# Kernel tuning notes

Hardware: AMD Instinct MI355X
Metric: run time of the kernel (lower is better)

## Reference

```python
import jax, jax.numpy as jnp
import numpy as np

N_ENTITIES = 100000
N_EDGES = 1250000
N_RELATIONS = 32
D = 64


def setup_inputs() -> dict:
    key = jax.random.key(0)
    k1, k2, k3, k4 = jax.random.split(key, 4)
    entity_emb = jax.random.normal(k1, (N_ENTITIES, D), dtype=jnp.float32)
    edge_index = jax.random.randint(k2, (2, N_EDGES), 0, N_ENTITIES, dtype=jnp.int64)
    edge_type = jax.random.randint(k3, (N_EDGES,), 0, N_RELATIONS, dtype=jnp.int64)
    weight = jax.random.normal(k4, (N_RELATIONS, D), dtype=jnp.float32)
    return {"entity_emb": entity_emb, "edge_index": edge_index,
            "edge_type": edge_type, "weight": weight}


def reference(entity_emb, edge_index, edge_type, weight):
    n_entities = entity_emb.shape[0]
    head, tail = edge_index[0], edge_index[1]
    # gather tail entity embeddings and relation embeddings, elementwise multiply
    neigh_relation_emb = entity_emb[tail] * weight[edge_type]  # [E, D]
    # scatter_mean by head index
    sums = jax.ops.segment_sum(neigh_relation_emb, head, num_segments=n_entities)
    counts = jax.ops.segment_sum(jnp.ones((head.shape[0],), dtype=entity_emb.dtype),
                                 head, num_segments=n_entities)
    entity_agg = sums / jnp.maximum(counts, 1.0)[:, None]  # empty segments -> 0
    return entity_agg
```

## Files before the change

kernel.cpp:

```cpp
#include <hip/hip_runtime.h>

#define D 64
#define BIN_SHIFT 7
#define BIN_SIZE 128
#define MAX_BINS 1024
#define BINCAP 2560
#define K1_THREADS 512
#define K1_EPT 8
#define K1_EPB (K1_THREADS * K1_EPT)
#define K2_THREADS 512
#define NREL 32


__global__ void __launch_bounds__(K1_THREADS)
bin_sort_kernel(const int* __restrict__ head,
                const int* __restrict__ tail,
                const int* __restrict__ etype,
                int* __restrict__ binCount,
                unsigned* __restrict__ recs,
                int nbins, int n_edges) {
    __shared__ int hist[MAX_BINS];
    __shared__ int pos[MAX_BINS];
    int tid = threadIdx.x;
    for (int b = tid; b < nbins; b += K1_THREADS) hist[b] = 0;
    __syncthreads();

    long blockBase = (long)blockIdx.x * K1_EPB;
    int hv[K1_EPT];
#pragma unroll
    for (int k = 0; k < K1_EPT; k++) {
        long e = blockBase + (long)k * K1_THREADS + tid;
        hv[k] = (e < n_edges) ? head[e] : -1;
        if (hv[k] >= 0) atomicAdd(&hist[hv[k] >> BIN_SHIFT], 1);
    }
    __syncthreads();

    for (int b = tid; b < nbins; b += K1_THREADS) {
        int c = hist[b];
        pos[b] = (c > 0) ? atomicAdd(&binCount[b], c) : 0;
    }
    __syncthreads();

#pragma unroll
    for (int k = 0; k < K1_EPT; k++) {
        int h = hv[k];
        if (h >= 0) {
            long e = blockBase + (long)k * K1_THREADS + tid;
            int b = h >> BIN_SHIFT;
            int r = atomicAdd(&pos[b], 1);
            if (r < BINCAP)
                recs[(long)b * BINCAP + r] =
                    (unsigned)tail[e] | ((unsigned)etype[e] << 17)
                  | ((unsigned)(h & (BIN_SIZE - 1)) << 22);
        }
    }
}

__global__ void __launch_bounds__(K2_THREADS)
aggregate_bin_kernel(const float* __restrict__ emb,
                     const float* __restrict__ weight,
                     const unsigned* __restrict__ recs,
                     const int* __restrict__ binCount,
                     float* __restrict__ out, int n_ent) {
    __shared__ unsigned raw[BINCAP];
    __shared__ unsigned sorted[BINCAP + 16];
    __shared__ float wlds[NREL * D];
    __shared__ int hist[BIN_SIZE];
    __shared__ int off[BIN_SIZE];
    __shared__ int cur[BIN_SIZE];

    int tid = threadIdx.x;
    int b = blockIdx.x;
    int n = min(binCount[b], BINCAP);

    for (int i = tid; i < BINCAP + 16; i += K2_THREADS) sorted[i] = 0u;
    for (int i = tid; i < NREL * D; i += K2_THREADS) wlds[i] = weight[i];
    if (tid < BIN_SIZE) hist[tid] = 0;
    __syncthreads();

    const unsigned* gr = recs + (long)b * BINCAP;
    for (int i = tid; i < n; i += K2_THREADS) {
        unsigned q = gr[i];
        raw[i] = q;
        atomicAdd(&hist[(q >> 22) & 127], 1);
    }
    __syncthreads();

    int v = 0;
    if (tid < BIN_SIZE) { v = hist[tid]; off[tid] = v; }
    __syncthreads();
    for (int s = 1; s < BIN_SIZE; s <<= 1) {
        int x = 0;
        if (tid < BIN_SIZE && tid >= s) x = off[tid - s];
        __syncthreads();
        if (tid < BIN_SIZE) off[tid] += x;
        __syncthreads();
    }
    if (tid < BIN_SIZE) { off[tid] -= v; cur[tid] = off[tid]; }
    __syncthreads();

    for (int i = tid; i < n; i += K2_THREADS) {
        unsigned q = raw[i];
        int p = atomicAdd(&cur[(q >> 22) & 127], 1);
        sorted[p] = q;
    }
    __syncthreads();

    int lane = tid & 63;
    int wave = tid >> 6;
    int g = lane >> 4;
    int c = lane & 15;
    int hbase = b << BIN_SHIFT;

    for (int hl = wave; hl < BIN_SIZE; hl += 8) {
        if (hbase + hl >= n_ent) break;
        int o = off[hl];
        int deg = hist[hl];
        float4 acc = make_float4(0.f, 0.f, 0.f, 0.f);
        for (int i = 0; i < deg; i += 16) {
            int e0 = i + g, e1 = i + 4 + g, e2 = i + 8 + g, e3 = i + 12 + g;
            unsigned q0 = sorted[o + e0];
            unsigned q1 = sorted[o + e1];
            unsigned q2 = sorted[o + e2];
            unsigned q3 = sorted[o + e3];
            float4 v0 = *(const float4*)&emb[(long)(q0 & 0x1FFFF) * D + c * 4];
            float4 v1 = *(const float4*)&emb[(long)(q1 & 0x1FFFF) * D + c * 4];
            float4 v2 = *(const float4*)&emb[(long)(q2 & 0x1FFFF) * D + c * 4];
            float4 v3 = *(const float4*)&emb[(long)(q3 & 0x1FFFF) * D + c * 4];
            float4 w0 = *(const float4*)&wlds[(((q0 >> 17) & 31) << 6) + c * 4];
            float4 w1 = *(const float4*)&wlds[(((q1 >> 17) & 31) << 6) + c * 4];
            float4 w2 = *(const float4*)&wlds[(((q2 >> 17) & 31) << 6) + c * 4];
            float4 w3 = *(const float4*)&wlds[(((q3 >> 17) & 31) << 6) + c * 4];
            float m0 = (e0 < deg) ? 1.f : 0.f;
            float m1 = (e1 < deg) ? 1.f : 0.f;
            float m2 = (e2 < deg) ? 1.f : 0.f;
            float m3 = (e3 < deg) ? 1.f : 0.f;
            acc.x += m0 * v0.x * w0.x; acc.y += m0 * v0.y * w0.y;
            acc.z += m0 * v0.z * w0.z; acc.w += m0 * v0.w * w0.w;
            acc.x += m1 * v1.x * w1.x; acc.y += m1 * v1.y * w1.y;
            acc.z += m1 * v1.z * w1.z; acc.w += m1 * v1.w * w1.w;
            acc.x += m2 * v2.x * w2.x; acc.y += m2 * v2.y * w2.y;
            acc.z += m2 * v2.z * w2.z; acc.w += m2 * v2.w * w2.w;
            acc.x += m3 * v3.x * w3.x; acc.y += m3 * v3.y * w3.y;
            acc.z += m3 * v3.z * w3.z; acc.w += m3 * v3.w * w3.w;
        }
        acc.x += __shfl_xor(acc.x, 16); acc.y += __shfl_xor(acc.y, 16);
        acc.z += __shfl_xor(acc.z, 16); acc.w += __shfl_xor(acc.w, 16);
        acc.x += __shfl_xor(acc.x, 32); acc.y += __shfl_xor(acc.y, 32);
        acc.z += __shfl_xor(acc.z, 32); acc.w += __shfl_xor(acc.w, 32);
        if (g == 0) {
            float inv = 1.f / fmaxf((float)deg, 1.f);
            *(float4*)&out[(long)(hbase + hl) * D + c * 4] =
                make_float4(acc.x * inv, acc.y * inv, acc.z * inv, acc.w * inv);
        }
    }
}

__global__ void fb_scatter(const float* __restrict__ emb, const int* __restrict__ head,
                           const int* __restrict__ tail, const int* __restrict__ etype,
                           const float* __restrict__ weight, float* __restrict__ out,
                           float* __restrict__ cnt, int n_edges) {
    int gtid = blockIdx.x * blockDim.x + threadIdx.x;
    int e = gtid >> 6, lane = threadIdx.x & 63;
    if (e >= n_edges) return;
    int h = head[e], t = tail[e], r = etype[e];
    atomicAdd(&out[(long)h * D + lane], emb[(long)t * D + lane] * weight[r * D + lane]);
    if (lane == 0) atomicAdd(&cnt[h], 1.0f);
}
__global__ void fb_divide(float* __restrict__ out, const float* __restrict__ cnt, int n) {
    int i = blockIdx.x * blockDim.x + threadIdx.x;
    if (i < n) out[i] = out[i] / fmaxf(cnt[i >> 6], 1.0f);
}


extern "C" void kernel_launch(void* const* d_in, const int* in_sizes, int n_in,
                              void* d_out, int out_size, void* d_ws, size_t ws_size,
                              hipStream_t stream) {
    const float* emb    = (const float*)d_in[0];
    const int*   eidx   = (const int*)  d_in[1];
    const int*   etype  = (const int*)  d_in[2];
    const float* weight = (const float*)d_in[3];
    float* out = (float*)d_out;

    int n_edges = in_sizes[2];
    int n_ent   = out_size / D;
    const int* head = eidx;
    const int* tail = eidx + n_edges;

    int nbins = (n_ent + BIN_SIZE - 1) >> BIN_SHIFT;
    size_t need = sizeof(int) * ((size_t)nbins * (BINCAP + 1));
    long mean_load = (n_ent > 0) ? ((long)n_edges * BIN_SIZE / n_ent) : 0;
    bool ok = (n_ent <= 131072) && (nbins <= MAX_BINS) && (ws_size >= need) &&
              (mean_load + 700 <= BINCAP);

    if (ok) {
        int* binCount  = (int*)d_ws;
        unsigned* recs = (unsigned*)(binCount + nbins);

        hipMemsetAsync(binCount, 0, (size_t)nbins * sizeof(int), stream);

        int nblocks = (n_edges + K1_EPB - 1) / K1_EPB;
        bin_sort_kernel<<<nblocks, K1_THREADS, 0, stream>>>(
            head, tail, etype, binCount, recs, nbins, n_edges);

        aggregate_bin_kernel<<<nbins, K2_THREADS, 0, stream>>>(
            emb, weight, recs, binCount, out, n_ent);
    } else {
        float* cnt = (float*)d_ws;
        hipMemsetAsync(out, 0, (size_t)out_size * sizeof(float), stream);
        hipMemsetAsync(cnt, 0, (size_t)n_ent * sizeof(float), stream);
        long tt = (long)n_edges * 64;
        fb_scatter<<<(int)((tt + 255) / 256), 256, 0, stream>>>(
            emb, head, tail, etype, weight, out, cnt, n_edges);
        fb_divide<<<(out_size + 255) / 256, 256, 0, stream>>>(out, cnt, out_size);
    }
}
```

Measured before the change: 158.4 us.

## Stage bin records in LDS for coalesced writes and split aggregation into half-bins

The binning kernel now sorts each block's records by bin in shared memory. It then writes them to global memory contiguously, using a binary search over bin bases, instead of as scattered per-edge stores. The aggregation kernel launches two 256-thread blocks per bin, each handling 64 heads, which doubles the block count for better occupancy. Each wave now processes two heads at once to expose more independent gathers. In exchange, each half-block rescans the whole bin's records, there is an extra LDS prefix scan, and a second capacity limit (HCAP) can push more inputs onto the fallback path.

```diff
diff --git a/kernel.cpp b/kernel.cpp
--- a/kernel.cpp
+++ b/kernel.cpp
@@ -5,10 +5,11 @@
 #define BIN_SIZE 128
 #define MAX_BINS 1024
 #define BINCAP 2560
+#define HCAP 1536
 #define K1_THREADS 512
 #define K1_EPT 8
 #define K1_EPB (K1_THREADS * K1_EPT)
-#define K2_THREADS 512
+#define K2_THREADS 256
 #define NREL 32
 
 
@@ -19,139 +20,211 @@
                 int* __restrict__ binCount,
                 unsigned* __restrict__ recs,
                 int nbins, int n_edges) {
+    __shared__ unsigned srec[K1_EPB];
     __shared__ int hist[MAX_BINS];
-    __shared__ int pos[MAX_BINS];
+    __shared__ int base[MAX_BINS + 1];
+    __shared__ int cur[MAX_BINS];
+    __shared__ int gpos[MAX_BINS];
+    __shared__ int tmp[K1_THREADS];
+
     int tid = threadIdx.x;
-    for (int b = tid; b < nbins; b += K1_THREADS) hist[b] = 0;
+    for (int b = tid; b < MAX_BINS; b += K1_THREADS) hist[b] = 0;
     __syncthreads();
 
     long blockBase = (long)blockIdx.x * K1_EPB;
-    int hv[K1_EPT];
+    int nvalid = (int)(((long)n_edges - blockBase < (long)K1_EPB)
+                       ? ((long)n_edges - blockBase) : (long)K1_EPB);
+
+    unsigned rv[K1_EPT]; int bv[K1_EPT];
 #pragma unroll
     for (int k = 0; k < K1_EPT; k++) {
         long e = blockBase + (long)k * K1_THREADS + tid;
-        hv[k] = (e < n_edges) ? head[e] : -1;
-        if (hv[k] >= 0) atomicAdd(&hist[hv[k] >> BIN_SHIFT], 1);
-    }
+        if (e < n_edges) {
+            int h = head[e];
+            bv[k] = h >> BIN_SHIFT;
+            rv[k] = (unsigned)tail[e] | ((unsigned)etype[e] << 17)
+                  | ((unsigned)(h & (BIN_SIZE - 1)) << 22);
+            atomicAdd(&hist[bv[k]], 1);
+        } else bv[k] = -1;
+    }
+    __syncthreads();
+
+    int s0 = hist[2 * tid], s1 = hist[2 * tid + 1];
+    tmp[tid] = s0 + s1;
+    __syncthreads();
+    for (int s = 1; s < K1_THREADS; s <<= 1) {
+        int x = (tid >= s) ? tmp[tid - s] : 0;
+        __syncthreads();
+        tmp[tid] += x;
+        __syncthreads();
+    }
+    int pairExcl = tmp[tid] - (s0 + s1);
+    base[2 * tid] = pairExcl;      cur[2 * tid] = pairExcl;
+    base[2 * tid + 1] = pairExcl + s0; cur[2 * tid + 1] = pairExcl + s0;
+    if (tid == K1_THREADS - 1) base[MAX_BINS] = tmp[tid];
     __syncthreads();
 
     for (int b = tid; b < nbins; b += K1_THREADS) {
         int c = hist[b];
-        pos[b] = (c > 0) ? atomicAdd(&binCount[b], c) : 0;
+        gpos[b] = (c > 0) ? atomicAdd(&binCount[b], c) : 0;
     }
     __syncthreads();
 
 #pragma unroll
     for (int k = 0; k < K1_EPT; k++) {
-        int h = hv[k];
-        if (h >= 0) {
-            long e = blockBase + (long)k * K1_THREADS + tid;
-            int b = h >> BIN_SHIFT;
-            int r = atomicAdd(&pos[b], 1);
-            if (r < BINCAP)
-                recs[(long)b * BINCAP + r] =
-                    (unsigned)tail[e] | ((unsigned)etype[e] << 17)
-                  | ((unsigned)(h & (BIN_SIZE - 1)) << 22);
-        }
+        if (bv[k] >= 0) {
+            int p = atomicAdd(&cur[bv[k]], 1);
+            srec[p] = rv[k];
+        }
+    }
+    __syncthreads();
+
+    for (int i = tid; i < nvalid; i += K1_THREADS) {
+        int lo = 0, hi = nbins - 1;
+        while (lo < hi) {
+            int mid = (lo + hi + 1) >> 1;
+            if (base[mid] <= i) lo = mid; else hi = mid - 1;
+        }
+        int b = lo;
+        int off = gpos[b] + (i - base[b]);
+        if (off < BINCAP)
+            recs[(long)b * BINCAP + off] = srec[i];
     }
 }
 
 __global__ void __launch_bounds__(K2_THREADS)
-aggregate_bin_kernel(const float* __restrict__ emb,
-                     const float* __restrict__ weight,
-                     const unsigned* __restrict__ recs,
-                     const int* __restrict__ binCount,
-                     float* __restrict__ out, int n_ent) {
-    __shared__ unsigned raw[BINCAP];
-    __shared__ unsigned sorted[BINCAP + 16];
+aggregate_half_kernel(const float* __restrict__ emb,
+                      const float* __restrict__ weight,
+                      const unsigned* __restrict__ recs,
+                      const int* __restrict__ binCount,
+                      float* __restrict__ out, int n_ent) {
+    __shared__ unsigned raw[HCAP];
+    __shared__ unsigned sorted[HCAP + 16];
     __shared__ float wlds[NREL * D];
-    __shared__ int hist[BIN_SIZE];
-    __shared__ int off[BIN_SIZE];
-    __shared__ int cur[BIN_SIZE];
+    __shared__ int hist[64], off[64], cur[64];
+    __shared__ int nh;
 
     int tid = threadIdx.x;
-    int b = blockIdx.x;
+    int b = blockIdx.x >> 1;
+    int half = blockIdx.x & 1;
     int n = min(binCount[b], BINCAP);
 
-    for (int i = tid; i < BINCAP + 16; i += K2_THREADS) sorted[i] = 0u;
+    for (int i = tid; i < HCAP + 16; i += K2_THREADS) sorted[i] = 0u;
     for (int i = tid; i < NREL * D; i += K2_THREADS) wlds[i] = weight[i];
-    if (tid < BIN_SIZE) hist[tid] = 0;
+    if (tid < 64) hist[tid] = 0;
+    if (tid == 0) nh = 0;
     __syncthreads();
 
     const unsigned* gr = recs + (long)b * BINCAP;
     for (int i = tid; i < n; i += K2_THREADS) {
         unsigned q = gr[i];
-        raw[i] = q;
-        atomicAdd(&hist[(q >> 22) & 127], 1);
-    }
-    __syncthreads();
+        int hl = (q >> 22) & 127;
+        if ((hl >> 6) == half) {
+            int p = atomicAdd(&nh, 1);
+            if (p < HCAP) { raw[p] = q; atomicAdd(&hist[hl & 63], 1); }
+        }
+    }
+    __syncthreads();
+    int m = min(nh, HCAP);
 
     int v = 0;
-    if (tid < BIN_SIZE) { v = hist[tid]; off[tid] = v; }
-    __syncthreads();
-    for (int s = 1; s < BIN_SIZE; s <<= 1) {
+    if (tid < 64) { v = hist[tid]; off[tid] = v; }
+    __syncthreads();
+    for (int s = 1; s < 64; s <<= 1) {
         int x = 0;
-        if (tid < BIN_SIZE && tid >= s) x = off[tid - s];
-        __syncthreads();
-        if (tid < BIN_SIZE) off[tid] += x;
-        __syncthreads();
-    }
-    if (tid < BIN_SIZE) { off[tid] -= v; cur[tid] = off[tid]; }
-    __syncthreads();
-
-    for (int i = tid; i < n; i += K2_THREADS) {
+        if (tid < 64 && tid >= s) x = off[tid - s];
+        __syncthreads();
+        if (tid < 64) off[tid] += x;
+        __syncthreads();
+    }
+    if (tid < 64) { off[tid] -= v; cur[tid] = off[tid]; }
+    __syncthreads();
+
+    for (int i = tid; i < m; i += K2_THREADS) {
         unsigned q = raw[i];
-        int p = atomicAdd(&cur[(q >> 22) & 127], 1);
+        int p = atomicAdd(&cur[(q >> 22) & 63], 1);
         sorted[p] = q;
     }
     __syncthreads();
 
-    int lane = tid & 63;
-    int wave = tid >> 6;
-    int g = lane >> 4;
-    int c = lane & 15;
-    int hbase = b << BIN_SHIFT;
-
-    for (int hl = wave; hl < BIN_SIZE; hl += 8) {
-        if (hbase + hl >= n_ent) break;
-        int o = off[hl];
-        int deg = hist[hl];
-        float4 acc = make_float4(0.f, 0.f, 0.f, 0.f);
-        for (int i = 0; i < deg; i += 16) {
+    int lane = tid & 63, wave = tid >> 6;
+    int g = lane >> 4, c = lane & 15;
+    int hbase = (b << BIN_SHIFT) + (half << 6);
+    int cap = m + 15;
+
+    for (int j = 0; j < 16; j += 2) {
+        int hA = wave * 16 + j, hB = hA + 1;
+        int oA = off[hA], dA = hist[hA];
+        int oB = off[hB], dB = hist[hB];
+        float4 aA = make_float4(0.f,0.f,0.f,0.f);
+        float4 aB = make_float4(0.f,0.f,0.f,0.f);
+        int dmax = max(dA, dB);
+        for (int i = 0; i < dmax; i += 16) {
             int e0 = i + g, e1 = i + 4 + g, e2 = i + 8 + g, e3 = i + 12 + g;
-            unsigned q0 = sorted[o + e0];
-            unsigned q1 = sorted[o + e1];
-            unsigned q2 = sorted[o + e2];
-            unsigned q3 = sorted[o + e3];
-            float4 v0 = *(const float4*)&emb[(long)(q0 & 0x1FFFF) * D + c * 4];
-            float4 v1 = *(const float4*)&emb[(long)(q1 & 0x1FFFF) * D + c * 4];
-            float4 v2 = *(const float4*)&emb[(long)(q2 & 0x1FFFF) * D + c * 4];
-            float4 v3 = *(const float4*)&emb[(long)(q3 & 0x1FFFF) * D + c * 4];
-            float4 w0 = *(const float4*)&wlds[(((q0 >> 17) & 31) << 6) + c * 4];
-            float4 w1 = *(const float4*)&wlds[(((q1 >> 17) & 31) << 6) + c * 4];
-            float4 w2 = *(const float4*)&wlds[(((q2 >> 17) & 31) << 6) + c * 4];
-            float4 w3 = *(const float4*)&wlds[(((q3 >> 17) & 31) << 6) + c * 4];
-            float m0 = (e0 < deg) ? 1.f : 0.f;
-            float m1 = (e1 < deg) ? 1.f : 0.f;
-            float m2 = (e2 < deg) ? 1.f : 0.f;
-            float m3 = (e3 < deg) ? 1.f : 0.f;
-            acc.x += m0 * v0.x * w0.x; acc.y += m0 * v0.y * w0.y;
-            acc.z += m0 * v0.z * w0.z; acc.w += m0 * v0.w * w0.w;
-            acc.x += m1 * v1.x * w1.x; acc.y += m1 * v1.y * w1.y;
-            acc.z += m1 * v1.z * w1.z; acc.w += m1 * v1.w * w1.w;
-            acc.x += m2 * v2.x * w2.x; acc.y += m2 * v2.y * w2.y;
-            acc.z += m2 * v2.z * w2.z; acc.w += m2 * v2.w * w2.w;
-            acc.x += m3 * v3.x * w3.x; acc.y += m3 * v3.y * w3.y;
-            acc.z += m3 * v3.z * w3.z; acc.w += m3 * v3.w * w3.w;
-        }
-        acc.x += __shfl_xor(acc.x, 16); acc.y += __shfl_xor(acc.y, 16);
-        acc.z += __shfl_xor(acc.z, 16); acc.w += __shfl_xor(acc.w, 16);
-        acc.x += __shfl_xor(acc.x, 32); acc.y += __shfl_xor(acc.y, 32);
-        acc.z += __shfl_xor(acc.z, 32); acc.w += __shfl_xor(acc.w, 32);
+            unsigned qa0 = sorted[min(oA + e0, cap)];
+            unsigned qa1 = sorted[min(oA + e1, cap)];
+            unsigned qa2 = sorted[min(oA + e2, cap)];
+            unsigned qa3 = sorted[min(oA + e3, cap)];
+            unsigned qb0 = sorted[min(oB + e0, cap)];
+            unsigned qb1 = sorted[min(oB + e1, cap)];
+            unsigned qb2 = sorted[min(oB + e2, cap)];
+            unsigned qb3 = sorted[min(oB + e3, cap)];
+            float4 va0 = *(const float4*)&emb[(long)(qa0 & 0x1FFFF) * D + c * 4];
+            float4 va1 = *(const float4*)&emb[(long)(qa1 & 0x1FFFF) * D + c * 4];
+            float4 va2 = *(const float4*)&emb[(long)(qa2 & 0x1FFFF) * D + c * 4];
+            float4 va3 = *(const float4*)&emb[(long)(qa3 & 0x1FFFF) * D + c * 4];
+            float4 vb0 = *(const float4*)&emb[(long)(qb0 & 0x1FFFF) * D + c * 4];
+            float4 vb1 = *(const float4*)&emb[(long)(qb1 & 0x1FFFF) * D + c * 4];
+            float4 vb2 = *(const float4*)&emb[(long)(qb2 & 0x1FFFF) * D + c * 4];
+            float4 vb3 = *(const float4*)&emb[(long)(qb3 & 0x1FFFF) * D + c * 4];
+            float4 wa0 = *(const float4*)&wlds[(((qa0 >> 17) & 31) << 6) + c * 4];
+            float4 wa1 = *(const float4*)&wlds[(((qa1 >> 17) & 31) << 6) + c * 4];
+            float4 wa2 = *(const float4*)&wlds[(((qa2 >> 17) & 31) << 6) + c * 4];
+            float4 wa3 = *(const float4*)&wlds[(((qa3 >> 17) & 31) << 6) + c * 4];
+            float4 wb0 = *(const float4*)&wlds[(((qb0 >> 17) & 31) << 6) + c * 4];
+            float4 wb1 = *(const float4*)&wlds[(((qb1 >> 17) & 31) << 6) + c * 4];
+            float4 wb2 = *(const float4*)&wlds[(((qb2 >> 17) & 31) << 6) + c * 4];
+            float4 wb3 = *(const float4*)&wlds[(((qb3 >> 17) & 31) << 6) + c * 4];
+            float ma0 = (e0 < dA) ? 1.f : 0.f, mb0 = (e0 < dB) ? 1.f : 0.f;
+            float ma1 = (e1 < dA) ? 1.f : 0.f, mb1 = (e1 < dB) ? 1.f : 0.f;
+            float ma2 = (e2 < dA) ? 1.f : 0.f, mb2 = (e2 < dB) ? 1.f : 0.f;
+            float ma3 = (e3 < dA) ? 1.f : 0.f, mb3 = (e3 < dB) ? 1.f : 0.f;
+            aA.x += ma0*va0.x*wa0.x; aA.y += ma0*va0.y*wa0.y;
+            aA.z += ma0*va0.z*wa0.z; aA.w += ma0*va0.w*wa0.w;
+            aA.x += ma1*va1.x*wa1.x; aA.y += ma1*va1.y*wa1.y;
+            aA.z += ma1*va1.z*wa1.z; aA.w += ma1*va1.w*wa1.w;
+            aA.x += ma2*va2.x*wa2.x; aA.y += ma2*va2.y*wa2.y;
+            aA.z += ma2*va2.z*wa2.z; aA.w += ma2*va2.w*wa2.w;
+            aA.x += ma3*va3.x*wa3.x; aA.y += ma3*va3.y*wa3.y;
+            aA.z += ma3*va3.z*wa3.z; aA.w += ma3*va3.w*wa3.w;
+            aB.x += mb0*vb0.x*wb0.x; aB.y += mb0*vb0.y*wb0.y;
+            aB.z += mb0*vb0.z*wb0.z; aB.w += mb0*vb0.w*wb0.w;
+            aB.x += mb1*vb1.x*wb1.x; aB.y += mb1*vb1.y*wb1.y;
+            aB.z += mb1*vb1.z*wb1.z; aB.w += mb1*vb1.w*wb1.w;
+            aB.x += mb2*vb2.x*wb2.x; aB.y += mb2*vb2.y*wb2.y;
+            aB.z += mb2*vb2.z*wb2.z; aB.w += mb2*vb2.w*wb2.w;
+            aB.x += mb3*vb3.x*wb3.x; aB.y += mb3*vb3.y*wb3.y;
+            aB.z += mb3*vb3.z*wb3.z; aB.w += mb3*vb3.w*wb3.w;
+        }
+        aA.x += __shfl_xor(aA.x, 16); aA.y += __shfl_xor(aA.y, 16);
+        aA.z += __shfl_xor(aA.z, 16); aA.w += __shfl_xor(aA.w, 16);
+        aA.x += __shfl_xor(aA.x, 32); aA.y += __shfl_xor(aA.y, 32);
+        aA.z += __shfl_xor(aA.z, 32); aA.w += __shfl_xor(aA.w, 32);
+        aB.x += __shfl_xor(aB.x, 16); aB.y += __shfl_xor(aB.y, 16);
+        aB.z += __shfl_xor(aB.z, 16); aB.w += __shfl_xor(aB.w, 16);
+        aB.x += __shfl_xor(aB.x, 32); aB.y += __shfl_xor(aB.y, 32);
+        aB.z += __shfl_xor(aB.z, 32); aB.w += __shfl_xor(aB.w, 32);
         if (g == 0) {
-            float inv = 1.f / fmaxf((float)deg, 1.f);
-            *(float4*)&out[(long)(hbase + hl) * D + c * 4] =
-                make_float4(acc.x * inv, acc.y * inv, acc.z * inv, acc.w * inv);
+            if (hbase + hA < n_ent) {
+                float inv = 1.f / fmaxf((float)dA, 1.f);
+                *(float4*)&out[(long)(hbase + hA) * D + c * 4] =
+                    make_float4(aA.x*inv, aA.y*inv, aA.z*inv, aA.w*inv);
+            }
+            if (hbase + hB < n_ent) {
+                float inv = 1.f / fmaxf((float)dB, 1.f);
+                *(float4*)&out[(long)(hbase + hB) * D + c * 4] =
+                    make_float4(aB.x*inv, aB.y*inv, aB.z*inv, aB.w*inv);
+            }
         }
     }
 }
@@ -190,8 +263,9 @@
     int nbins = (n_ent + BIN_SIZE - 1) >> BIN_SHIFT;
     size_t need = sizeof(int) * ((size_t)nbins * (BINCAP + 1));
     long mean_load = (n_ent > 0) ? ((long)n_edges * BIN_SIZE / n_ent) : 0;
+    long mean_half = mean_load / 2;
     bool ok = (n_ent <= 131072) && (nbins <= MAX_BINS) && (ws_size >= need) &&
-              (mean_load + 700 <= BINCAP);
+              (mean_load + 700 <= BINCAP) && (mean_half + 400 <= HCAP);
 
     if (ok) {
         int* binCount  = (int*)d_ws;
@@ -203,7 +277,7 @@
         bin_sort_kernel<<<nblocks, K1_THREADS, 0, stream>>>(
             head, tail, etype, binCount, recs, nbins, n_edges);
 
-        aggregate_bin_kernel<<<nbins, K2_THREADS, 0, stream>>>(
+        aggregate_half_kernel<<<nbins * 2, K2_THREADS, 0, stream>>>(
             emb, weight, recs, binCount, out, n_ent);
     } else {
         float* cnt = (float*)d_ws;
```

New measurement: 159.7 us. Within noise of the previous version (+0.9%).

## Gather bf16 embeddings and stage bin records in LDS for coalesced writes

Applied to the files above, without the earlier changes.

Adds a pre-pass that converts the fp32 entity embeddings to bf16 and also zeroes the bin counters, replacing the memset. The aggregate kernel then gathers half-width rows to cut random-gather traffic. The bin sort kernel now sorts each block's records locally in LDS by bin, using a prefix scan and a binary search per record, so the global writes to each bin are contiguous instead of scattered. This costs an extra full read/write pass over the embedding table, bf16 rounding error in the output, and more LDS and synchronisation in the sort kernel.

```diff
diff --git a/kernel.cpp b/kernel.cpp
--- a/kernel.cpp
+++ b/kernel.cpp
@@ -12,6 +12,26 @@
 #define NREL 32
 
 
+__device__ __forceinline__ float bf2f(unsigned short u) {
+    union { unsigned i; float f; } x; x.i = ((unsigned)u) << 16; return x.f;
+}
+
+__global__ void cvt_kernel(const float* __restrict__ emb,
+                           unsigned short* __restrict__ emb16,
+                           int* __restrict__ binCount, int nbins, long n4) {
+    long i = (long)blockIdx.x * blockDim.x + threadIdx.x;
+    if (i < (long)nbins) binCount[i] = 0;
+    if (i >= n4) return;
+    float4 v = ((const float4*)emb)[i];
+    ushort4 o;
+    unsigned b;
+    b = __float_as_uint(v.x); o.x = (unsigned short)((b + 0x7FFF + ((b >> 16) & 1)) >> 16);
+    b = __float_as_uint(v.y); o.y = (unsigned short)((b + 0x7FFF + ((b >> 16) & 1)) >> 16);
+    b = __float_as_uint(v.z); o.z = (unsigned short)((b + 0x7FFF + ((b >> 16) & 1)) >> 16);
+    b = __float_as_uint(v.w); o.w = (unsigned short)((b + 0x7FFF + ((b >> 16) & 1)) >> 16);
+    ((ushort4*)emb16)[i] = o;
+}
+
 __global__ void __launch_bounds__(K1_THREADS)
 bin_sort_kernel(const int* __restrict__ head,
                 const int* __restrict__ tail,
@@ -19,45 +39,80 @@
                 int* __restrict__ binCount,
                 unsigned* __restrict__ recs,
                 int nbins, int n_edges) {
+    __shared__ unsigned srec[K1_EPB];
     __shared__ int hist[MAX_BINS];
-    __shared__ int pos[MAX_BINS];
+    __shared__ int base[MAX_BINS + 1];
+    __shared__ int cur[MAX_BINS];
+    __shared__ int gpos[MAX_BINS];
+    __shared__ int tmp[K1_THREADS];
+
     int tid = threadIdx.x;
-    for (int b = tid; b < nbins; b += K1_THREADS) hist[b] = 0;
+    for (int b = tid; b < MAX_BINS; b += K1_THREADS) hist[b] = 0;
     __syncthreads();
 
     long blockBase = (long)blockIdx.x * K1_EPB;
-    int hv[K1_EPT];
+    int nvalid = (int)(((long)n_edges - blockBase < (long)K1_EPB)
+                       ? ((long)n_edges - blockBase) : (long)K1_EPB);
+
+    unsigned rv[K1_EPT]; int bv[K1_EPT];
 #pragma unroll
     for (int k = 0; k < K1_EPT; k++) {
         long e = blockBase + (long)k * K1_THREADS + tid;
-        hv[k] = (e < n_edges) ? head[e] : -1;
-        if (hv[k] >= 0) atomicAdd(&hist[hv[k] >> BIN_SHIFT], 1);
-    }
+        if (e < n_edges) {
+            int h = head[e];
+            bv[k] = h >> BIN_SHIFT;
+            rv[k] = (unsigned)tail[e] | ((unsigned)etype[e] << 17)
+                  | ((unsigned)(h & (BIN_SIZE - 1)) << 22);
+            atomicAdd(&hist[bv[k]], 1);
+        } else bv[k] = -1;
+    }
+    __syncthreads();
+
+    int s0 = hist[2 * tid], s1 = hist[2 * tid + 1];
+    tmp[tid] = s0 + s1;
+    __syncthreads();
+    for (int s = 1; s < K1_THREADS; s <<= 1) {
+        int x = (tid >= s) ? tmp[tid - s] : 0;
+        __syncthreads();
+        tmp[tid] += x;
+        __syncthreads();
+    }
+    int pairExcl = tmp[tid] - (s0 + s1);
+    base[2 * tid] = pairExcl;          cur[2 * tid] = pairExcl;
+    base[2 * tid + 1] = pairExcl + s0; cur[2 * tid + 1] = pairExcl + s0;
+    if (tid == K1_THREADS - 1) base[MAX_BINS] = tmp[tid];
     __syncthreads();
 
     for (int b = tid; b < nbins; b += K1_THREADS) {
         int c = hist[b];
-        pos[b] = (c > 0) ? atomicAdd(&binCount[b], c) : 0;
+        gpos[b] = (c > 0) ? atomicAdd(&binCount[b], c) : 0;
     }
     __syncthreads();
 
 #pragma unroll
     for (int k = 0; k < K1_EPT; k++) {
-        int h = hv[k];
-        if (h >= 0) {
-            long e = blockBase + (long)k * K1_THREADS + tid;
-            int b = h >> BIN_SHIFT;
-            int r = atomicAdd(&pos[b], 1);
-            if (r < BINCAP)
-                recs[(long)b * BINCAP + r] =
-                    (unsigned)tail[e] | ((unsigned)etype[e] << 17)
-                  | ((unsigned)(h & (BIN_SIZE - 1)) << 22);
-        }
+        if (bv[k] >= 0) {
+            int p = atomicAdd(&cur[bv[k]], 1);
+            srec[p] = rv[k];
+        }
+    }
+    __syncthreads();
+
+    for (int i = tid; i < nvalid; i += K1_THREADS) {
+        int lo = 0, hi = nbins - 1;
+        while (lo < hi) {
+            int mid = (lo + hi + 1) >> 1;
+            if (base[mid] <= i) lo = mid; else hi = mid - 1;
+        }
+        int b = lo;
+        int off = gpos[b] + (i - base[b]);
+        if (off < BINCAP)
+            recs[(long)b * BINCAP + off] = srec[i];
     }
 }
 
 __global__ void __launch_bounds__(K2_THREADS)
-aggregate_bin_kernel(const float* __restrict__ emb,
+aggregate_bin_kernel(const unsigned short* __restrict__ emb16,
                      const float* __restrict__ weight,
                      const unsigned* __restrict__ recs,
                      const int* __restrict__ binCount,
@@ -123,10 +178,10 @@
             unsigned q1 = sorted[o + e1];
             unsigned q2 = sorted[o + e2];
             unsigned q3 = sorted[o + e3];
-            float4 v0 = *(const float4*)&emb[(long)(q0 & 0x1FFFF) * D + c * 4];
-            float4 v1 = *(const float4*)&emb[(long)(q1 & 0x1FFFF) * D + c * 4];
-            float4 v2 = *(const float4*)&emb[(long)(q2 & 0x1FFFF) * D + c * 4];
-            float4 v3 = *(const float4*)&emb[(long)(q3 & 0x1FFFF) * D + c * 4];
+            ushort4 u0 = *(const ushort4*)&emb16[(long)(q0 & 0x1FFFF) * D + c * 4];
+            ushort4 u1 = *(const ushort4*)&emb16[(long)(q1 & 0x1FFFF) * D + c * 4];
+            ushort4 u2 = *(const ushort4*)&emb16[(long)(q2 & 0x1FFFF) * D + c * 4];
+            ushort4 u3 = *(const ushort4*)&emb16[(long)(q3 & 0x1FFFF) * D + c * 4];
             float4 w0 = *(const float4*)&wlds[(((q0 >> 17) & 31) << 6) + c * 4];
             float4 w1 = *(const float4*)&wlds[(((q1 >> 17) & 31) << 6) + c * 4];
             float4 w2 = *(const float4*)&wlds[(((q2 >> 17) & 31) << 6) + c * 4];
@@ -135,14 +190,14 @@
             float m1 = (e1 < deg) ? 1.f : 0.f;
             float m2 = (e2 < deg) ? 1.f : 0.f;
             float m3 = (e3 < deg) ? 1.f : 0.f;
-            acc.x += m0 * v0.x * w0.x; acc.y += m0 * v0.y * w0.y;
-            acc.z += m0 * v0.z * w0.z; acc.w += m0 * v0.w * w0.w;
-            acc.x += m1 * v1.x * w1.x; acc.y += m1 * v1.y * w1.y;
-            acc.z += m1 * v1.z * w1.z; acc.w += m1 * v1.w * w1.w;
-            acc.x += m2 * v2.x * w2.x; acc.y += m2 * v2.y * w2.y;
-            acc.z += m2 * v2.z * w2.z; acc.w += m2 * v2.w * w2.w;
-            acc.x += m3 * v3.x * w3.x; acc.y += m3 * v3.y * w3.y;
-            acc.z += m3 * v3.z * w3.z; acc.w += m3 * v3.w * w3.w;
+            acc.x += m0 * bf2f(u0.x) * w0.x; acc.y += m0 * bf2f(u0.y) * w0.y;
+            acc.z += m0 * bf2f(u0.z) * w0.z; acc.w += m0 * bf2f(u0.w) * w0.w;
+            acc.x += m1 * bf2f(u1.x) * w1.x; acc.y += m1 * bf2f(u1.y) * w1.y;
+            acc.z += m1 * bf2f(u1.z) * w1.z; acc.w += m1 * bf2f(u1.w) * w1.w;
+            acc.x += m2 * bf2f(u2.x) * w2.x; acc.y += m2 * bf2f(u2.y) * w2.y;
+            acc.z += m2 * bf2f(u2.z) * w2.z; acc.w += m2 * bf2f(u2.w) * w2.w;
+            acc.x += m3 * bf2f(u3.x) * w3.x; acc.y += m3 * bf2f(u3.y) * w3.y;
+            acc.z += m3 * bf2f(u3.z) * w3.z; acc.w += m3 * bf2f(u3.w) * w3.w;
         }
         acc.x += __shfl_xor(acc.x, 16); acc.y += __shfl_xor(acc.y, 16);
         acc.z += __shfl_xor(acc.z, 16); acc.w += __shfl_xor(acc.w, 16);
@@ -188,7 +243,10 @@
     const int* tail = eidx + n_edges;
 
     int nbins = (n_ent + BIN_SIZE - 1) >> BIN_SHIFT;
-    size_t need = sizeof(int) * ((size_t)nbins * (BINCAP + 1));
+    size_t recs_bytes = sizeof(int) * ((size_t)nbins * BINCAP);
+    size_t cnt_bytes  = sizeof(int) * (size_t)nbins;
+    size_t emb16_off  = (cnt_bytes + recs_bytes + 15) & ~((size_t)15);
+    size_t need = emb16_off + (size_t)n_ent * D * sizeof(unsigned short);
     long mean_load = (n_ent > 0) ? ((long)n_edges * BIN_SIZE / n_ent) : 0;
     bool ok = (n_ent <= 131072) && (nbins <= MAX_BINS) && (ws_size >= need) &&
               (mean_load + 700 <= BINCAP);
@@ -196,15 +254,18 @@
     if (ok) {
         int* binCount  = (int*)d_ws;
         unsigned* recs = (unsigned*)(binCount + nbins);
-
-        hipMemsetAsync(binCount, 0, (size_t)nbins * sizeof(int), stream);
+        unsigned short* emb16 = (unsigned short*)((char*)d_ws + emb16_off);
+
+        long n4 = (long)n_ent * D / 4;
+        cvt_kernel<<<(int)((n4 + 255) / 256), 256, 0, stream>>>(
+            emb, emb16, binCount, nbins, n4);
 
         int nblocks = (n_edges + K1_EPB - 1) / K1_EPB;
         bin_sort_kernel<<<nblocks, K1_THREADS, 0, stream>>>(
             head, tail, etype, binCount, recs, nbins, n_edges);
 
         aggregate_bin_kernel<<<nbins, K2_THREADS, 0, stream>>>(
-            emb, weight, recs, binCount, out, n_ent);
+            emb16, weight, recs, binCount, out, n_ent);
     } else {
         float* cnt = (float*)d_ws;
         hipMemsetAsync(out, 0, (size_t)out_size * sizeof(float), stream);
```

After: 157.1 us. No clear change (-0.8%).
